# Performance work log

Measured on AMD Instinct MI355X. Metric: run time of the kernel, lower is better.

The kernel has to match this reference:

```python
import jax, jax.numpy as jnp
import numpy as np

D = 256      # d_model
H = 8        # n_heads
L = 4        # n_levels
P = 4        # n_points
DFF = 1024   # d_ffn
DH = D // H  # head dim
SPATIAL = np.array([[100, 100], [50, 50], [25, 25], [13, 13]], dtype=np.int64)  # (H_l, W_l)
LV = int((SPATIAL[:, 0] * SPATIAL[:, 1]).sum())  # 13294 flattened memory tokens


def layer_norm(x, w, b, eps=1e-5):
    m = jnp.mean(x, -1, keepdims=True)
    v = jnp.mean((x - m) ** 2, -1, keepdims=True)
    return (x - m) * jax.lax.rsqrt(v + eps) * w + b


def setup_inputs() -> dict:
    key = jax.random.key(0)
    ks = jax.random.split(key, 16)
    nq, bs = 900, 8

    def w(k, shape, s=0.02):
        return jax.random.normal(k, shape, dtype=jnp.float32) * s

    return {
        "tgt": jax.random.normal(ks[0], (nq, bs, D), jnp.float32),
        "tgt_query_pos": jax.random.normal(ks[1], (nq, bs, D), jnp.float32),
        "tgt_reference_points": jax.random.uniform(ks[2], (nq, bs, L, 2), jnp.float32),
        "memory": jax.random.normal(ks[3], (LV, bs, D), jnp.float32),
        "sa_Wqkv": w(ks[4], (3 * D, D)), "sa_bqkv": jnp.zeros((3 * D,), jnp.float32),
        "sa_Wo": w(ks[5], (D, D)), "sa_bo": jnp.zeros((D,), jnp.float32),
        "ln1_w": jnp.ones((D,), jnp.float32), "ln1_b": jnp.zeros((D,), jnp.float32),
        "ln2_w": jnp.ones((D,), jnp.float32), "ln2_b": jnp.zeros((D,), jnp.float32),
        "ln3_w": jnp.ones((D,), jnp.float32), "ln3_b": jnp.zeros((D,), jnp.float32),
        "ca_Woff": w(ks[6], (H * L * P * 2, D)), "ca_boff": w(ks[7], (H * L * P * 2,), 0.5),
        "ca_Wattn": w(ks[8], (H * L * P, D)), "ca_battn": jnp.zeros((H * L * P,), jnp.float32),
        "ca_Wval": w(ks[9], (D, D)), "ca_bval": jnp.zeros((D,), jnp.float32),
        "ca_Wout": w(ks[10], (D, D)), "ca_bout": jnp.zeros((D,), jnp.float32),
        "ffn_W1": w(ks[11], (DFF, D)), "ffn_b1": jnp.zeros((DFF,), jnp.float32),
        "ffn_W2": w(ks[12], (D, DFF)), "ffn_b2": jnp.zeros((D,), jnp.float32),
        "memory_key_padding_mask": jnp.zeros((bs, LV), jnp.bool_),
        "memory_spatial_shapes": jnp.asarray(SPATIAL),
    }


def msdeform_attn(query, ref, value, mask, shapes_np,
                  Woff, boff, Wattn, battn, Wval, bval, Wout, bout):
    # query: [bs,nq,D], ref: [bs,nq,L,2], value: [bs,lv,D], mask: [bs,lv]
    bs, nq, _ = query.shape
    lv = value.shape[1]
    v = value @ Wval.T + bval
    v = jnp.where(mask[:, :, None], 0.0, v)
    v = v.reshape(bs, lv, H, DH).transpose(0, 2, 1, 3)  # [bs,H,lv,DH]
    off = (query @ Woff.T + boff).reshape(bs, nq, H, L, P, 2)
    aw = jax.nn.softmax((query @ Wattn.T + battn).reshape(bs, nq, H, L * P), -1)
    aw = aw.reshape(bs, nq, H, L, P)
    # offset normalizer is [W_l, H_l]
    norm = jnp.asarray(shapes_np[:, ::-1].copy(), jnp.float32)  # [L,2]
    loc = ref[:, :, None, :, None, :] + off / norm[None, None, None, :, None, :]
    out = jnp.zeros((bs, nq, H, DH), jnp.float32)
    start = 0
    for l in range(L):
        Hl, Wl = int(shapes_np[l, 0]), int(shapes_np[l, 1])
        vf = v[:, :, start:start + Hl * Wl]  # [bs,H,Hl*Wl,DH]
        start += Hl * Wl
        # grid_sample(align_corners=False) pixel coords
        x = loc[:, :, :, l, :, 0] * Wl - 0.5  # [bs,nq,H,P]
        y = loc[:, :, :, l, :, 1] * Hl - 0.5
        x0 = jnp.floor(x); y0 = jnp.floor(y)
        fx = x - x0; fy = y - y0
        x0i = x0.astype(jnp.int32); y0i = y0.astype(jnp.int32)

        def gather(yi, xi):
            valid = ((xi >= 0) & (xi < Wl) & (yi >= 0) & (yi < Hl)).astype(jnp.float32)
            idx = jnp.clip(yi, 0, Hl - 1) * Wl + jnp.clip(xi, 0, Wl - 1)
            idx_t = idx.transpose(0, 2, 1, 3).reshape(bs, H, nq * P, 1)
            g = jnp.take_along_axis(vf, idx_t, axis=2)  # [bs,H,nq*P,DH]
            return g * valid.transpose(0, 2, 1, 3).reshape(bs, H, nq * P, 1)

        def wgt(w):
            return w.transpose(0, 2, 1, 3).reshape(bs, H, nq * P, 1)

        samp = (gather(y0i, x0i) * wgt((1 - fx) * (1 - fy))
                + gather(y0i, x0i + 1) * wgt(fx * (1 - fy))
                + gather(y0i + 1, x0i) * wgt((1 - fx) * fy)
                + gather(y0i + 1, x0i + 1) * wgt(fx * fy))
        samp = samp.reshape(bs, H, nq, P, DH)
        out = out + jnp.einsum('bhqpd,bqhp->bqhd', samp, aw[:, :, :, l])
    return out.reshape(bs, nq, D) @ Wout.T + bout


def reference(tgt, tgt_query_pos, tgt_reference_points, memory,
              sa_Wqkv, sa_bqkv, sa_Wo, sa_bo,
              ln1_w, ln1_b, ln2_w, ln2_b, ln3_w, ln3_b,
              ca_Woff, ca_boff, ca_Wattn, ca_battn, ca_Wval, ca_bval, ca_Wout, ca_bout,
              ffn_W1, ffn_b1, ffn_W2, ffn_b2,
              memory_key_padding_mask, memory_spatial_shapes):
    shapes_np = np.asarray(memory_spatial_shapes)  # static per trace
    nq, bs, _ = tgt.shape
    # --- self attention (post-LN, residual) ---
    q = tgt + tgt_query_pos
    qp = (q @ sa_Wqkv[:D].T + sa_bqkv[:D]).reshape(nq, bs, H, DH)
    kp = (q @ sa_Wqkv[D:2 * D].T + sa_bqkv[D:2 * D]).reshape(nq, bs, H, DH)
    vp = (tgt @ sa_Wqkv[2 * D:].T + sa_bqkv[2 * D:]).reshape(nq, bs, H, DH)
    scores = jnp.einsum('qbhd,kbhd->bhqk', qp, kp) * (1.0 / float(np.sqrt(DH)))
    attn = jax.nn.softmax(scores, -1)
    o = jnp.einsum('bhqk,kbhd->qbhd', attn, vp).reshape(nq, bs, D) @ sa_Wo.T + sa_bo
    tgt = layer_norm(tgt + o, ln2_w, ln2_b)
    # --- multi-scale deformable cross attention ---
    query = (tgt + tgt_query_pos).transpose(1, 0, 2)      # [bs,nq,D]
    ref = tgt_reference_points.transpose(1, 0, 2, 3)      # [bs,nq,L,2]
    val = memory.transpose(1, 0, 2)                       # [bs,lv,D]
    ca = msdeform_attn(query, ref, val, memory_key_padding_mask, shapes_np,
                       ca_Woff, ca_boff, ca_Wattn, ca_battn,
                       ca_Wval, ca_bval, ca_Wout, ca_bout).transpose(1, 0, 2)
    tgt = layer_norm(tgt + ca, ln1_w, ln1_b)
    # --- FFN ---
    t2 = jax.nn.relu(tgt @ ffn_W1.T + ffn_b1) @ ffn_W2.T + ffn_b2
    return layer_norm(tgt + t2, ln3_w, ln3_b)
```

## Files before the change

kernel.cpp:

```cpp
#include <hip/hip_runtime.h>
#include <hip/hip_bf16.h>

#define NQ   900
#define BSZ  8
#define DM   256
#define NH   8
#define DHD  32
#define DFF_ 1024
#define LVTOT 13294
#define NTOK (NQ*BSZ)
#define MVAL (LVTOT*BSZ)

typedef __attribute__((ext_vector_type(8))) short bf16x8;
typedef __attribute__((ext_vector_type(4))) short bf16x4;
typedef __attribute__((ext_vector_type(4))) float f32x4;
typedef unsigned int u32;

__device__ __forceinline__ unsigned short f2bf(float x) {
  union { __hip_bfloat16 h; unsigned short u; } cv;
  cv.h = __float2bfloat16(x);
  return cv.u;
}
__device__ __forceinline__ float bf2f(unsigned short u) {
  union { __hip_bfloat16 h; unsigned short u; } cv;
  cv.u = u;
  return __bfloat162float(cv.h);
}

__device__ __forceinline__ void gl_lds16(const void* gsrc, void* ldst) {
  __builtin_amdgcn_global_load_lds(
      (const __attribute__((address_space(1))) u32*)gsrc,
      (__attribute__((address_space(3))) u32*)ldst, 16, 0, 0);
}

__global__ __launch_bounds__(256) void addcast_kernel(const float* __restrict__ a,
                                                      const float* __restrict__ b,
                                                      unsigned short* __restrict__ o, int n8) {
  int i = blockIdx.x * 256 + threadIdx.x;
  if (i >= n8) return;
  float4 a0 = ((const float4*)a)[i * 2], a1 = ((const float4*)a)[i * 2 + 1];
  float4 b0 = ((const float4*)b)[i * 2], b1 = ((const float4*)b)[i * 2 + 1];
  bf16x8 v;
  v[0] = (short)f2bf(a0.x + b0.x); v[1] = (short)f2bf(a0.y + b0.y);
  v[2] = (short)f2bf(a0.z + b0.z); v[3] = (short)f2bf(a0.w + b0.w);
  v[4] = (short)f2bf(a1.x + b1.x); v[5] = (short)f2bf(a1.y + b1.y);
  v[6] = (short)f2bf(a1.z + b1.z); v[7] = (short)f2bf(a1.w + b1.w);
  *(bf16x8*)(o + (long)i * 8) = v;
}

__global__ __launch_bounds__(256) void cast_weights_kernel(
    const float* p0, const float* p1, const float* p2, const float* p3,
    const float* p4, const float* p5, const float* p6, const float* p7,
    unsigned short* dst) {
  long i8 = ((long)blockIdx.x * 256 + threadIdx.x) * 8;
  if (i8 >= 1015808) return;
  const float* src; long off;
  if      (i8 < 196608) { src = p0; off = i8; }
  else if (i8 < 262144) { src = p1; off = i8 - 196608; }
  else if (i8 < 327680) { src = p2; off = i8 - 262144; }
  else if (i8 < 393216) { src = p3; off = i8 - 327680; }
  else if (i8 < 425984) { src = p4; off = i8 - 393216; }
  else if (i8 < 491520) { src = p5; off = i8 - 425984; }
  else if (i8 < 753664) { src = p6; off = i8 - 491520; }
  else                  { src = p7; off = i8 - 753664; }
  float4 a = *(const float4*)(src + off);
  float4 b = *(const float4*)(src + off + 4);
  bf16x8 v;
  v[0] = (short)f2bf(a.x); v[1] = (short)f2bf(a.y);
  v[2] = (short)f2bf(a.z); v[3] = (short)f2bf(a.w);
  v[4] = (short)f2bf(b.x); v[5] = (short)f2bf(b.y);
  v[6] = (short)f2bf(b.z); v[7] = (short)f2bf(b.w);
  *(bf16x8*)(dst + i8) = v;
}

__global__ __launch_bounds__(256) void concat_bias_kernel(const float* __restrict__ a,
                                                          const float* __restrict__ b,
                                                          float* __restrict__ o) {
  int i = blockIdx.x * 256 + threadIdx.x;
  if (i < 256) o[i] = a[i];
  else if (i < 384) o[i] = b[i - 256];
}

template <int AF32, int OUT_BF16, int RELU, int NT>
__global__ __launch_bounds__(256) void gemm_mfma_kernel(
    const void* __restrict__ Araw, const unsigned short* __restrict__ W,
    const float* __restrict__ bias, void* __restrict__ C,
    int M, int ldc) {
  constexpr int K = NT * 32;
  constexpr int ABYTES = AF32 ? 16384 : 8192;
  __shared__ alignas(16) unsigned char As0[ABYTES];
  __shared__ alignas(16) unsigned char As1[ABYTES];
  __shared__ alignas(16) unsigned char As2[ABYTES];
  __shared__ alignas(16) unsigned char Bs0[8192];
  __shared__ alignas(16) unsigned char Bs1[8192];
  __shared__ alignas(16) unsigned char Bs2[8192];
  int tid = threadIdx.x;
  int l = tid & 63, w = tid >> 6;
  int lr = l & 15, lg = l >> 4;
  int wr = w >> 1, wc = w & 1;
  int n0 = blockIdx.x * 128, m0 = blockIdx.y * 128;

  f32x4 acc[4][4];
#pragma unroll
  for (int m = 0; m < 4; m++)
#pragma unroll
    for (int n = 0; n < 4; n++) acc[m][n] = (f32x4){0.f, 0.f, 0.f, 0.f};

  auto stage = [&](unsigned char* Ab, unsigned char* Bb, int k0) {
#pragma unroll
    for (int i = 0; i < 2; i++) {
      int c16 = i * 4 + w;
      int row = c16 * 16 + (l >> 2);
      int sc = (l & 3) ^ (row & 3);
      gl_lds16(W + (long)(n0 + row) * K + k0 + sc * 8, Bb + c16 * 1024 + l * 16);
    }
    if (AF32) {
      const float* Af = (const float*)Araw;
#pragma unroll
      for (int i = 0; i < 4; i++) {
        int c8 = i * 4 + w;
        int row = c8 * 8 + (l >> 3);
        int g = m0 + row; if (g >= M) g = M - 1;
        int sc = (l & 7) ^ (row & 7);
        gl_lds16(Af + (long)g * K + k0 + sc * 4, Ab + c8 * 1024 + l * 16);
      }
    } else {
      const unsigned short* A = (const unsigned short*)Araw;
#pragma unroll
      for (int i = 0; i < 2; i++) {
        int c16 = i * 4 + w;
        int row = c16 * 16 + (l >> 2);
        int g = m0 + row; if (g >= M) g = M - 1;
        int sc = (l & 3) ^ (row & 3);
        gl_lds16(A + (long)g * K + k0 + sc * 8, Ab + c16 * 1024 + l * 16);
      }
    }
  };

  auto compute = [&](const unsigned char* Ab, const unsigned char* Bb) {
    bf16x8 af[4], bfr[4];
    if (AF32) {
#pragma unroll
      for (int m = 0; m < 4; m++) {
        int row = wr * 64 + m * 16 + lr;
        f32x4 fa = *(const f32x4*)(Ab + row * 128 + (((lg * 2)     ^ (lr & 7)) * 16));
        f32x4 fb = *(const f32x4*)(Ab + row * 128 + (((lg * 2 + 1) ^ (lr & 7)) * 16));
        bf16x8 v;
        v[0] = (short)f2bf(fa[0]); v[1] = (short)f2bf(fa[1]);
        v[2] = (short)f2bf(fa[2]); v[3] = (short)f2bf(fa[3]);
        v[4] = (short)f2bf(fb[0]); v[5] = (short)f2bf(fb[1]);
        v[6] = (short)f2bf(fb[2]); v[7] = (short)f2bf(fb[3]);
        af[m] = v;
      }
    } else {
#pragma unroll
      for (int m = 0; m < 4; m++) {
        int row = wr * 64 + m * 16 + lr;
        af[m] = *(const bf16x8*)(Ab + row * 64 + ((lg ^ (lr & 3)) * 16));
      }
    }
#pragma unroll
    for (int n = 0; n < 4; n++) {
      int row = wc * 64 + n * 16 + lr;
      bfr[n] = *(const bf16x8*)(Bb + row * 64 + ((lg ^ (lr & 3)) * 16));
    }
#pragma unroll
    for (int m = 0; m < 4; m++)
#pragma unroll
      for (int n = 0; n < 4; n++)
        acc[m][n] = __builtin_amdgcn_mfma_f32_16x16x32_bf16(af[m], bfr[n], acc[m][n], 0, 0, 0);
  };

  unsigned char* Abuf[3] = {As0, As1, As2};
  unsigned char* Bbuf[3] = {Bs0, Bs1, Bs2};
  stage(As0, Bs0, 0);
  stage(As1, Bs1, 32);
  stage(As2, Bs2, 64);

#pragma unroll
  for (int t = 0; t < NT; t++) {
    const int ahead = NT - 1 - t;
    if (ahead >= 2) {
      if (AF32) asm volatile("s_waitcnt vmcnt(12)" ::: "memory");
      else      asm volatile("s_waitcnt vmcnt(8)"  ::: "memory");
    } else if (ahead == 1) {
      if (AF32) asm volatile("s_waitcnt vmcnt(6)" ::: "memory");
      else      asm volatile("s_waitcnt vmcnt(4)" ::: "memory");
    } else {
      asm volatile("s_waitcnt vmcnt(0)" ::: "memory");
    }
    __builtin_amdgcn_s_barrier();
    __builtin_amdgcn_sched_barrier(0);
    compute(Abuf[t % 3], Bbuf[t % 3]);
    __builtin_amdgcn_sched_barrier(0);
    __builtin_amdgcn_s_barrier();
    __builtin_amdgcn_sched_barrier(0);
    if (t + 3 < NT) stage(Abuf[t % 3], Bbuf[t % 3], (t + 3) * 32);
  }

  float bv[4];
#pragma unroll
  for (int ni = 0; ni < 4; ni++) bv[ni] = bias[n0 + wc * 64 + ni * 16 + lr];
#pragma unroll
  for (int mi = 0; mi < 4; mi++) {
#pragma unroll
    for (int r = 0; r < 4; r++) {
      int row = m0 + wr * 64 + mi * 16 + lg * 4 + r;
      if (row < M) {
#pragma unroll
        for (int ni = 0; ni < 4; ni++) {
          int col = n0 + wc * 64 + ni * 16 + lr;
          float v = acc[mi][ni][r] + bv[ni];
          if (RELU) v = fmaxf(v, 0.f);
          if (OUT_BF16) ((unsigned short*)C)[(long)row * ldc + col] = f2bf(v);
          else          ((float*)C)[(long)row * ldc + col] = v;
        }
      }
    }
  }
}

__global__ __launch_bounds__(256) void attn_mfma_kernel(const unsigned short* __restrict__ qkv,
                                                        unsigned short* __restrict__ out) {
  __shared__ unsigned short Vt[32][72];
  __shared__ unsigned short Ps[4][16][72];
  int tid = threadIdx.x;
  int l = tid & 63, w = tid >> 6;
  int lr = l & 15, lg = l >> 4;
  int q0 = blockIdx.x * 64;
  int h = blockIdx.y & 7, b = blockIdx.y >> 3;
  const float scale = 0.17677669529663687f;

  int qrow = q0 + w * 16 + lr;
  int qclamp = qrow < 899 ? qrow : 899;
  bf16x8 qf = *(const bf16x8*)(qkv + ((long)qclamp * 8 + b) * 768 + h * 32 + lg * 8);

  f32x4 o_acc[2];
  o_acc[0] = (f32x4){0.f, 0.f, 0.f, 0.f};
  o_acc[1] = (f32x4){0.f, 0.f, 0.f, 0.f};
  float m_run[4] = {-1e30f, -1e30f, -1e30f, -1e30f};
  float l_run[4] = {0.f, 0.f, 0.f, 0.f};

  for (int k0 = 0; k0 < NQ; k0 += 64) {
    __syncthreads();
    {
      int key = tid >> 2, dg = tid & 3;
      int kk = k0 + key; if (kk > 899) kk = 899;
      bf16x8 vv = *(const bf16x8*)(qkv + ((long)kk * 8 + b) * 768 + 512 + h * 32 + dg * 8);
#pragma unroll
      for (int j = 0; j < 8; j++) Vt[dg * 8 + j][key] = (unsigned short)vv[j];
    }
    f32x4 sg[4];
#pragma unroll
    for (int ng = 0; ng < 4; ng++) {
      int key = k0 + ng * 16 + lr; int kc = key < 899 ? key : 899;
      bf16x8 kf = *(const bf16x8*)(qkv + ((long)kc * 8 + b) * 768 + 256 + h * 32 + lg * 8);
      sg[ng] = __builtin_amdgcn_mfma_f32_16x16x32_bf16(qf, kf, (f32x4){0.f, 0.f, 0.f, 0.f}, 0, 0, 0);
    }
    float sv[4][4];
#pragma unroll
    for (int ng = 0; ng < 4; ng++) {
      bool bad = (k0 + ng * 16 + lr) >= NQ;
#pragma unroll
      for (int r = 0; r < 4; r++) sv[ng][r] = bad ? -1e30f : sg[ng][r] * scale;
    }
    float p[4][4];
#pragma unroll
    for (int r = 0; r < 4; r++) {
      float rmax = fmaxf(fmaxf(sv[0][r], sv[1][r]), fmaxf(sv[2][r], sv[3][r]));
#pragma unroll
      for (int mk = 8; mk; mk >>= 1) rmax = fmaxf(rmax, __shfl_xor(rmax, mk));
      float mnew = fmaxf(m_run[r], rmax);
      float fs = __expf(m_run[r] - mnew);
      m_run[r] = mnew;
      float ps = 0.f;
#pragma unroll
      for (int ng = 0; ng < 4; ng++) { p[ng][r] = __expf(sv[ng][r] - mnew); ps += p[ng][r]; }
#pragma unroll
      for (int mk = 8; mk; mk >>= 1) ps += __shfl_xor(ps, mk);
      l_run[r] = l_run[r] * fs + ps;
      o_acc[0][r] *= fs;
      o_acc[1][r] *= fs;
    }
#pragma unroll
    for (int ng = 0; ng < 4; ng++)
#pragma unroll
      for (int r = 0; r < 4; r++)
        Ps[w][lg * 4 + r][lr + ng * 16] = f2bf(p[ng][r]);
    __syncthreads();
#pragma unroll
    for (int ks = 0; ks < 2; ks++) {
      bf16x8 pf = *(const bf16x8*)&Ps[w][lr][ks * 32 + lg * 8];
#pragma unroll
      for (int ni = 0; ni < 2; ni++) {
        bf16x8 vf = *(const bf16x8*)&Vt[ni * 16 + lr][ks * 32 + lg * 8];
        o_acc[ni] = __builtin_amdgcn_mfma_f32_16x16x32_bf16(pf, vf, o_acc[ni], 0, 0, 0);
      }
    }
  }
#pragma unroll
  for (int r = 0; r < 4; r++) {
    int orow = q0 + w * 16 + lg * 4 + r;
    if (orow < NQ) {
      float inv = 1.f / l_run[r];
      unsigned short* op = out + ((long)orow * 8 + b) * 256 + h * 32 + lr;
      op[0]  = f2bf(o_acc[0][r] * inv);
      op[16] = f2bf(o_acc[1][r] * inv);
    }
  }
}

__device__ __forceinline__ void fetch8_acc(const unsigned short* __restrict__ vtmp, int lo, int W,
                                           int yi, int xi, int b, int col0, float wgt,
                                           float* a) {
  if ((xi < 0) | (xi >= W) | (yi < 0) | (yi >= W)) return;
  const unsigned short* p = vtmp + ((long)((lo + yi * W + xi) * BSZ + b)) * 256 + col0;
  bf16x8 r = *(const bf16x8*)p;
#pragma unroll
  for (int j = 0; j < 8; j++) a[j] += wgt * bf2f((unsigned short)r[j]);
}

__global__ __launch_bounds__(256) void sampler_kernel(const unsigned short* __restrict__ vtmp,
                                                      const float* __restrict__ oa,
                                                      const float* __restrict__ ref,
                                                      unsigned short* __restrict__ samp) {
  __shared__ float s_off[8][256];
  __shared__ float s_aw[8][128];
  __shared__ float s_ref[8][8];
  int tid = threadIdx.x;
  int t0 = blockIdx.x * 8;
#pragma unroll
  for (int k = 0; k < 8; k++) s_off[k][tid] = oa[(long)(t0 + k) * 384 + tid];
#pragma unroll
  for (int i = 0; i < 4; i++) {
    int idx = i * 256 + tid;
    int k = idx >> 7, c = idx & 127;
    s_aw[k][c] = oa[(long)(t0 + k) * 384 + 256 + c];
  }
  if (tid < 64) s_ref[tid >> 3][tid & 7] = ref[(long)(t0 + (tid >> 3)) * 8 + (tid & 7)];
  __syncthreads();
  if (tid < 64) {
    int k = tid >> 3, hh = tid & 7;
    float* p = &s_aw[k][hh * 16];
    float m = -1e30f;
#pragma unroll
    for (int j = 0; j < 16; j++) m = fmaxf(m, p[j]);
    float s = 0.f;
#pragma unroll
    for (int j = 0; j < 16; j++) { p[j] = __expf(p[j] - m); s += p[j]; }
    float inv = 1.f / s;
#pragma unroll
    for (int j = 0; j < 16; j++) p[j] *= inv;
  }
  __syncthreads();
  int w = tid >> 5;
  int l = tid & 31;
  int t = t0 + w;
  int h = l >> 2, col0 = h * 32 + (l & 3) * 8;
  int b = t & 7;
  const int Wls[4]  = {100, 50, 25, 13};
  const int lofs[4] = {0, 10000, 12500, 13125};
  float a[8];
#pragma unroll
  for (int j = 0; j < 8; j++) a[j] = 0.f;
#pragma unroll
  for (int lvl = 0; lvl < 4; lvl++) {
    int W = Wls[lvl];
    float Wf = (float)W;
    int lo = lofs[lvl];
    float rx = s_ref[w][lvl * 2 + 0], ry = s_ref[w][lvl * 2 + 1];
#pragma unroll
    for (int p = 0; p < 4; p++) {
      float ox = s_off[w][((h * 4 + lvl) * 4 + p) * 2 + 0];
      float oy = s_off[w][((h * 4 + lvl) * 4 + p) * 2 + 1];
      float x = rx * Wf + ox - 0.5f;
      float y = ry * Wf + oy - 0.5f;
      float x0f = floorf(x), y0f = floorf(y);
      float fx = x - x0f, fy = y - y0f;
      int x0 = (int)x0f, y0 = (int)y0f;
      float aa = s_aw[w][h * 16 + lvl * 4 + p];
      float w00 = aa * (1.f - fx) * (1.f - fy);
      float w01 = aa * fx * (1.f - fy);
      float w10 = aa * (1.f - fx) * fy;
      float w11 = aa * fx * fy;
      fetch8_acc(vtmp, lo, W, y0,     x0,     b, col0, w00, a);
      fetch8_acc(vtmp, lo, W, y0,     x0 + 1, b, col0, w01, a);
      fetch8_acc(vtmp, lo, W, y0 + 1, x0,     b, col0, w10, a);
      fetch8_acc(vtmp, lo, W, y0 + 1, x0 + 1, b, col0, w11, a);
    }
  }
  bf16x8 o;
#pragma unroll
  for (int j = 0; j < 8; j++) o[j] = (short)f2bf(a[j]);
  *(bf16x8*)(samp + (long)t * 256 + col0) = o;
}

__global__ __launch_bounds__(256) void ln_kernel(const float* __restrict__ x,
                                                 const float* __restrict__ res,
                                                 const float* __restrict__ w,
                                                 const float* __restrict__ bvec,
                                                 float* __restrict__ out,
                                                 unsigned short* __restrict__ out_bf,
                                                 const float* __restrict__ pos,
                                                 unsigned short* __restrict__ pos_bf,
                                                 int rows) {
  int wv = threadIdx.x >> 6, lane = threadIdx.x & 63;
  int row = blockIdx.x * 4 + wv;
  if (row >= rows) return;
  float4 xv = *(const float4*)(x + (long)row * 256 + lane * 4);
  float4 rv = *(const float4*)(res + (long)row * 256 + lane * 4);
  float v0 = xv.x + rv.x, v1 = xv.y + rv.y, v2 = xv.z + rv.z, v3 = xv.w + rv.w;
  float s = v0 + v1 + v2 + v3;
#pragma unroll
  for (int o = 32; o; o >>= 1) s += __shfl_xor(s, o);
  float mean = s * (1.f / 256.f);
  float d0 = v0 - mean, d1 = v1 - mean, d2 = v2 - mean, d3 = v3 - mean;
  float q = d0 * d0 + d1 * d1 + d2 * d2 + d3 * d3;
#pragma unroll
  for (int o = 32; o; o >>= 1) q += __shfl_xor(q, o);
  float rstd = rsqrtf(q * (1.f / 256.f) + 1e-5f);
  float4 wv4 = *(const float4*)(w + lane * 4);
  float4 bv4 = *(const float4*)(bvec + lane * 4);
  float o0 = d0 * rstd * wv4.x + bv4.x;
  float o1 = d1 * rstd * wv4.y + bv4.y;
  float o2 = d2 * rstd * wv4.z + bv4.z;
  float o3 = d3 * rstd * wv4.w + bv4.w;
  *(float4*)(out + (long)row * 256 + lane * 4) = make_float4(o0, o1, o2, o3);
  if (out_bf) {
    unsigned short* p = out_bf + (long)row * 256 + lane * 4;
    p[0] = f2bf(o0); p[1] = f2bf(o1); p[2] = f2bf(o2); p[3] = f2bf(o3);
  }
  if (pos_bf) {
    float4 pv = *(const float4*)(pos + (long)row * 256 + lane * 4);
    unsigned short* p = pos_bf + (long)row * 256 + lane * 4;
    p[0] = f2bf(o0 + pv.x); p[1] = f2bf(o1 + pv.y);
    p[2] = f2bf(o2 + pv.z); p[3] = f2bf(o3 + pv.w);
  }
}

extern "C" void kernel_launch(void* const* d_in, const int* in_sizes, int n_in,
                              void* d_out, int out_size, void* d_ws, size_t ws_size,
                              hipStream_t stream) {
  const float* tgt     = (const float*)d_in[0];
  const float* pos     = (const float*)d_in[1];
  const float* refpts  = (const float*)d_in[2];
  const float* memory  = (const float*)d_in[3];
  const float* sa_Wqkv = (const float*)d_in[4];
  const float* sa_bqkv = (const float*)d_in[5];
  const float* sa_Wo   = (const float*)d_in[6];
  const float* sa_bo   = (const float*)d_in[7];
  const float* ln1_w   = (const float*)d_in[8];
  const float* ln1_b   = (const float*)d_in[9];
  const float* ln2_w   = (const float*)d_in[10];
  const float* ln2_b   = (const float*)d_in[11];
  const float* ln3_w   = (const float*)d_in[12];
  const float* ln3_b   = (const float*)d_in[13];
  const float* ca_Woff = (const float*)d_in[14];
  const float* ca_boff = (const float*)d_in[15];
  const float* ca_Wattn= (const float*)d_in[16];
  const float* ca_battn= (const float*)d_in[17];
  const float* ca_Wval = (const float*)d_in[18];
  const float* ca_bval = (const float*)d_in[19];
  const float* ca_Wout = (const float*)d_in[20];
  const float* ca_bout = (const float*)d_in[21];
  const float* ffn_W1  = (const float*)d_in[22];
  const float* ffn_b1  = (const float*)d_in[23];
  const float* ffn_W2  = (const float*)d_in[24];
  const float* ffn_b2  = (const float*)d_in[25];

  char* ws = (char*)d_ws;
  float*          buf_ca = (float*)(ws);
  float*          buf_t3 = (float*)(ws + 8388608);
  unsigned short* t3_bf  = (unsigned short*)(ws + 16777216);
  unsigned short* buf_h  = (unsigned short*)(ws + 20971520);
  float*          buf_f  = (float*)(ws + 36700160);
  float*          bias_cat = (float*)(ws + 44072960);
  unsigned short* buf_v  = (unsigned short*)(ws + 54452224);
  unsigned short* wts    = (unsigned short*)(ws + 112590848);
  unsigned short* buf_q  = (unsigned short*)(ws + 114622464);
  unsigned short* buf_qkv= (unsigned short*)(ws + 118308864);
  float*          buf_oa = (float*)(ws + 118308864);
  unsigned short* buf_o  = (unsigned short*)(ws + 129368064);
  unsigned short* buf_smp= (unsigned short*)(ws + 129368064);
  float*          buf_t2 = (float*)(ws + 133054464);

  const unsigned short* w_qkv = wts + 0;
  const unsigned short* w_o   = wts + 196608;
  const unsigned short* w_val = wts + 262144;
  const unsigned short* w_oa  = wts + 327680;
  const unsigned short* w_out = wts + 425984;
  const unsigned short* w_f1  = wts + 491520;
  const unsigned short* w_f2  = wts + 753664;

  dim3 blk(256);
  const int n8tok = NTOK * DM / 8;

  cast_weights_kernel<<<(1015808 / 8 + 255) / 256, blk, 0, stream>>>(
      sa_Wqkv, sa_Wo, ca_Wval, ca_Woff, ca_Wattn, ca_Wout, ffn_W1, ffn_W2, wts);
  concat_bias_kernel<<<2, blk, 0, stream>>>(ca_boff, ca_battn, bias_cat);
  addcast_kernel<<<(n8tok + 255) / 256, blk, 0, stream>>>(tgt, pos, buf_q, n8tok);
  gemm_mfma_kernel<0, 1, 0, 8><<<dim3(4, 57), blk, 0, stream>>>(buf_q, w_qkv, sa_bqkv,
                                                                buf_qkv, NTOK, 768);
  gemm_mfma_kernel<1, 1, 0, 8><<<dim3(2, 57), blk, 0, stream>>>(tgt, w_qkv + 512 * 256,
                                                                sa_bqkv + 512, buf_qkv + 512,
                                                                NTOK, 768);
  gemm_mfma_kernel<1, 1, 0, 8><<<dim3(2, 831), blk, 0, stream>>>(memory, w_val, ca_bval,
                                                                 buf_v, MVAL, 256);
  attn_mfma_kernel<<<dim3(15, 64), blk, 0, stream>>>(buf_qkv, buf_o);
  gemm_mfma_kernel<0, 0, 0, 8><<<dim3(2, 57), blk, 0, stream>>>(buf_o, w_o, sa_bo,
                                                                buf_t2, NTOK, 256);
  ln_kernel<<<1800, blk, 0, stream>>>(buf_t2, tgt, ln2_w, ln2_b, buf_t2, nullptr,
                                      pos, buf_q, NTOK);
  gemm_mfma_kernel<0, 0, 0, 8><<<dim3(3, 57), blk, 0, stream>>>(buf_q, w_oa, bias_cat,
                                                                buf_oa, NTOK, 384);
  sampler_kernel<<<NTOK / 8, blk, 0, stream>>>(buf_v, buf_oa, refpts, buf_smp);
  gemm_mfma_kernel<0, 0, 0, 8><<<dim3(2, 57), blk, 0, stream>>>(buf_smp, w_out, ca_bout,
                                                                buf_ca, NTOK, 256);
  ln_kernel<<<1800, blk, 0, stream>>>(buf_ca, buf_t2, ln1_w, ln1_b, buf_t3, t3_bf,
                                      nullptr, nullptr, NTOK);
  gemm_mfma_kernel<0, 1, 1, 8><<<dim3(8, 57), blk, 0, stream>>>(t3_bf, w_f1, ffn_b1,
                                                                buf_h, NTOK, 1024);
  gemm_mfma_kernel<0, 0, 0, 32><<<dim3(2, 57), blk, 0, stream>>>(buf_h, w_f2, ffn_b2,
                                                                 buf_f, NTOK, 256);
  ln_kernel<<<1800, blk, 0, stream>>>(buf_f, buf_t3, ln3_w, ln3_b, (float*)d_out, nullptr,
                                      nullptr, nullptr, NTOK);
}
```

Measured before the change: 234.9 us.

## Add K=256 GEMM kernel that preloads all weights to LDS and streams A

Introduces a GEMM kernel specialised for K=256 that loads the full 128x256 weight tile into LDS once, then reads A fragments directly from global memory into registers, with no A staging in LDS and no per-k-step barriers. It replaces the triple-buffered LDS pipeline for all K=256 GEMMs, including the large memory value projection. The aim is to remove the synchronisation and LDS traffic for A. The cost is 64KB of LDS per block, which limits occupancy, and uncoalesced direct global A loads whose latency is no longer hidden by a software pipeline.

```diff
diff --git a/kernel.cpp b/kernel.cpp
--- a/kernel.cpp
+++ b/kernel.cpp
@@ -79,6 +79,102 @@
   int i = blockIdx.x * 256 + threadIdx.x;
   if (i < 256) o[i] = a[i];
   else if (i < 384) o[i] = b[i - 256];
+}
+
+template <int AF32, int OUT_BF16, int RELU>
+__global__ __launch_bounds__(256, 2) void gemm_stream_kernel(
+    const void* __restrict__ Araw, const unsigned short* __restrict__ W,
+    const float* __restrict__ bias, void* __restrict__ C,
+    int M, int ldc) {
+  __shared__ alignas(16) unsigned char Bp[8][8192];
+  int tid = threadIdx.x;
+  int l = tid & 63, w = tid >> 6;
+  int lr = l & 15, lg = l >> 4;
+  int wr = w >> 1, wc = w & 1;
+  int n0 = blockIdx.x * 128, m0 = blockIdx.y * 128;
+
+#pragma unroll
+  for (int kt = 0; kt < 8; kt++) {
+#pragma unroll
+    for (int i = 0; i < 2; i++) {
+      int c16 = i * 4 + w;
+      int row = c16 * 16 + (l >> 2);
+      int sc = (l & 3) ^ (row & 3);
+      gl_lds16(W + (long)(n0 + row) * 256 + kt * 32 + sc * 8, Bp[kt] + c16 * 1024 + l * 16);
+    }
+  }
+
+  f32x4 acc[4][4];
+#pragma unroll
+  for (int m = 0; m < 4; m++)
+#pragma unroll
+    for (int n = 0; n < 4; n++) acc[m][n] = (f32x4){0.f, 0.f, 0.f, 0.f};
+
+  long arow[4];
+#pragma unroll
+  for (int m = 0; m < 4; m++) {
+    long r = m0 + wr * 64 + m * 16 + lr;
+    arow[m] = (r < M) ? r : (M - 1);
+  }
+
+  __syncthreads();
+
+#pragma unroll
+  for (int kt = 0; kt < 8; kt++) {
+    bf16x8 af[4];
+    if (AF32) {
+      const float* Af = (const float*)Araw;
+#pragma unroll
+      for (int m = 0; m < 4; m++) {
+        const float* p = Af + arow[m] * 256 + kt * 32 + lg * 8;
+        f32x4 fa = *(const f32x4*)p;
+        f32x4 fb = *(const f32x4*)(p + 4);
+        bf16x8 v;
+        v[0] = (short)f2bf(fa[0]); v[1] = (short)f2bf(fa[1]);
+        v[2] = (short)f2bf(fa[2]); v[3] = (short)f2bf(fa[3]);
+        v[4] = (short)f2bf(fb[0]); v[5] = (short)f2bf(fb[1]);
+        v[6] = (short)f2bf(fb[2]); v[7] = (short)f2bf(fb[3]);
+        af[m] = v;
+      }
+    } else {
+      const unsigned short* A = (const unsigned short*)Araw;
+#pragma unroll
+      for (int m = 0; m < 4; m++)
+        af[m] = *(const bf16x8*)(A + arow[m] * 256 + kt * 32 + lg * 8);
+    }
+    bf16x8 bfr[4];
+#pragma unroll
+    for (int n = 0; n < 4; n++) {
+      int row = wc * 64 + n * 16 + lr;
+      bfr[n] = *(const bf16x8*)(Bp[kt] + (row >> 4) * 1024 + ((row & 15) * 4 + (lg ^ (row & 3))) * 16);
+    }
+#pragma unroll
+    for (int m = 0; m < 4; m++)
+#pragma unroll
+      for (int n = 0; n < 4; n++)
+        acc[m][n] = __builtin_amdgcn_mfma_f32_16x16x32_bf16(af[m], bfr[n], acc[m][n], 0, 0, 0);
+  }
+
+  float bv[4];
+#pragma unroll
+  for (int ni = 0; ni < 4; ni++) bv[ni] = bias[n0 + wc * 64 + ni * 16 + lr];
+#pragma unroll
+  for (int mi = 0; mi < 4; mi++) {
+#pragma unroll
+    for (int r = 0; r < 4; r++) {
+      int row = m0 + wr * 64 + mi * 16 + lg * 4 + r;
+      if (row < M) {
+#pragma unroll
+        for (int ni = 0; ni < 4; ni++) {
+          int col = n0 + wc * 64 + ni * 16 + lr;
+          float v = acc[mi][ni][r] + bv[ni];
+          if (RELU) v = fmaxf(v, 0.f);
+          if (OUT_BF16) ((unsigned short*)C)[(long)row * ldc + col] = f2bf(v);
+          else          ((float*)C)[(long)row * ldc + col] = v;
+        }
+      }
+    }
+  }
 }
 
 template <int AF32, int OUT_BF16, int RELU, int NT>
@@ -499,27 +595,27 @@
       sa_Wqkv, sa_Wo, ca_Wval, ca_Woff, ca_Wattn, ca_Wout, ffn_W1, ffn_W2, wts);
   concat_bias_kernel<<<2, blk, 0, stream>>>(ca_boff, ca_battn, bias_cat);
   addcast_kernel<<<(n8tok + 255) / 256, blk, 0, stream>>>(tgt, pos, buf_q, n8tok);
-  gemm_mfma_kernel<0, 1, 0, 8><<<dim3(4, 57), blk, 0, stream>>>(buf_q, w_qkv, sa_bqkv,
-                                                                buf_qkv, NTOK, 768);
-  gemm_mfma_kernel<1, 1, 0, 8><<<dim3(2, 57), blk, 0, stream>>>(tgt, w_qkv + 512 * 256,
-                                                                sa_bqkv + 512, buf_qkv + 512,
-                                                                NTOK, 768);
-  gemm_mfma_kernel<1, 1, 0, 8><<<dim3(2, 831), blk, 0, stream>>>(memory, w_val, ca_bval,
-                                                                 buf_v, MVAL, 256);
+  gemm_stream_kernel<0, 1, 0><<<dim3(4, 57), blk, 0, stream>>>(buf_q, w_qkv, sa_bqkv,
+                                                               buf_qkv, NTOK, 768);
+  gemm_stream_kernel<1, 1, 0><<<dim3(2, 57), blk, 0, stream>>>(tgt, w_qkv + 512 * 256,
+                                                               sa_bqkv + 512, buf_qkv + 512,
+                                                               NTOK, 768);
+  gemm_stream_kernel<1, 1, 0><<<dim3(2, 831), blk, 0, stream>>>(memory, w_val, ca_bval,
+                                                                buf_v, MVAL, 256);
   attn_mfma_kernel<<<dim3(15, 64), blk, 0, stream>>>(buf_qkv, buf_o);
-  gemm_mfma_kernel<0, 0, 0, 8><<<dim3(2, 57), blk, 0, stream>>>(buf_o, w_o, sa_bo,
-                                                                buf_t2, NTOK, 256);
+  gemm_stream_kernel<0, 0, 0><<<dim3(2, 57), blk, 0, stream>>>(buf_o, w_o, sa_bo,
+                                                               buf_t2, NTOK, 256);
   ln_kernel<<<1800, blk, 0, stream>>>(buf_t2, tgt, ln2_w, ln2_b, buf_t2, nullptr,
                                       pos, buf_q, NTOK);
-  gemm_mfma_kernel<0, 0, 0, 8><<<dim3(3, 57), blk, 0, stream>>>(buf_q, w_oa, bias_cat,
-                                                                buf_oa, NTOK, 384);
+  gemm_stream_kernel<0, 0, 0><<<dim3(3, 57), blk, 0, stream>>>(buf_q, w_oa, bias_cat,
+                                                               buf_oa, NTOK, 384);
   sampler_kernel<<<NTOK / 8, blk, 0, stream>>>(buf_v, buf_oa, refpts, buf_smp);
-  gemm_mfma_kernel<0, 0, 0, 8><<<dim3(2, 57), blk, 0, stream>>>(buf_smp, w_out, ca_bout,
-                                                                buf_ca, NTOK, 256);
+  gemm_stream_kernel<0, 0, 0><<<dim3(2, 57), blk, 0, stream>>>(buf_smp, w_out, ca_bout,
+                                                               buf_ca, NTOK, 256);
   ln_kernel<<<1800, blk, 0, stream>>>(buf_ca, buf_t2, ln1_w, ln1_b, buf_t3, t3_bf,
                                       nullptr, nullptr, NTOK);
-  gemm_mfma_kernel<0, 1, 1, 8><<<dim3(8, 57), blk, 0, stream>>>(t3_bf, w_f1, ffn_b1,
-                                                                buf_h, NTOK, 1024);
+  gemm_stream_kernel<0, 1, 1><<<dim3(8, 57), blk, 0, stream>>>(t3_bf, w_f1, ffn_b1,
+                                                               buf_h, NTOK, 1024);
   gemm_mfma_kernel<0, 0, 0, 32><<<dim3(2, 57), blk, 0, stream>>>(buf_h, w_f2, ffn_b2,
                                                                  buf_f, NTOK, 256);
   ln_kernel<<<1800, blk, 0, stream>>>(buf_f, buf_t3, ln3_w, ln3_b, (float*)d_out, nullptr,
```

Measured after the change: 281.9 us. 1.2x slower.

## Replace triple-buffered GEMM pipeline with single-buffer 64-wide K steps

Applied to the files above, without the earlier changes.

The GEMM kernel drops its three-stage LDS ring buffer with hand-tuned vmcnt waits. It now uses one A/B buffer per block, loaded with K=64 per step and guarded by two __syncthreads per step, with __launch_bounds__(256,4) to raise occupancy. This trades intra-block load/compute overlap for more resident blocks and fewer barrier rounds, relying on other blocks to hide memory latency. The swizzle patterns are widened to 8/16 chunks to match the wider rows.

```diff
diff --git a/kernel.cpp b/kernel.cpp
--- a/kernel.cpp
+++ b/kernel.cpp
@@ -81,19 +81,15 @@
   else if (i < 384) o[i] = b[i - 256];
 }
 
-template <int AF32, int OUT_BF16, int RELU, int NT>
-__global__ __launch_bounds__(256) void gemm_mfma_kernel(
+template <int AF32, int OUT_BF16, int RELU, int NSTEP>
+__global__ __launch_bounds__(256, 4) void gemm_s_kernel(
     const void* __restrict__ Araw, const unsigned short* __restrict__ W,
     const float* __restrict__ bias, void* __restrict__ C,
     int M, int ldc) {
-  constexpr int K = NT * 32;
-  constexpr int ABYTES = AF32 ? 16384 : 8192;
-  __shared__ alignas(16) unsigned char As0[ABYTES];
-  __shared__ alignas(16) unsigned char As1[ABYTES];
-  __shared__ alignas(16) unsigned char As2[ABYTES];
-  __shared__ alignas(16) unsigned char Bs0[8192];
-  __shared__ alignas(16) unsigned char Bs1[8192];
-  __shared__ alignas(16) unsigned char Bs2[8192];
+  constexpr int K = NSTEP * 64;
+  constexpr int ABYTES = AF32 ? 32768 : 16384;
+  __shared__ alignas(16) unsigned char As[ABYTES];
+  __shared__ alignas(16) unsigned char Bs[16384];
   int tid = threadIdx.x;
   int l = tid & 63, w = tid >> 6;
   int lr = l & 15, lg = l >> 4;
@@ -106,96 +102,77 @@
 #pragma unroll
     for (int n = 0; n < 4; n++) acc[m][n] = (f32x4){0.f, 0.f, 0.f, 0.f};
 
-  auto stage = [&](unsigned char* Ab, unsigned char* Bb, int k0) {
-#pragma unroll
-    for (int i = 0; i < 2; i++) {
-      int c16 = i * 4 + w;
-      int row = c16 * 16 + (l >> 2);
-      int sc = (l & 3) ^ (row & 3);
-      gl_lds16(W + (long)(n0 + row) * K + k0 + sc * 8, Bb + c16 * 1024 + l * 16);
+  for (int t = 0; t < NSTEP; t++) {
+    int k0 = t * 64;
+    __syncthreads();
+#pragma unroll
+    for (int i4 = 0; i4 < 4; i4++) {
+      int i = i4 * 4 + w;
+      int row = i * 8 + (l >> 3);
+      int sc = (l & 7) ^ (row & 7);
+      gl_lds16(W + (long)(n0 + row) * K + k0 + sc * 8, Bs + i * 1024 + l * 16);
     }
     if (AF32) {
       const float* Af = (const float*)Araw;
 #pragma unroll
-      for (int i = 0; i < 4; i++) {
-        int c8 = i * 4 + w;
-        int row = c8 * 8 + (l >> 3);
+      for (int i4 = 0; i4 < 8; i4++) {
+        int i = i4 * 4 + w;
+        int row = i * 4 + (l >> 4);
         int g = m0 + row; if (g >= M) g = M - 1;
-        int sc = (l & 7) ^ (row & 7);
-        gl_lds16(Af + (long)g * K + k0 + sc * 4, Ab + c8 * 1024 + l * 16);
+        int sc = (l & 15) ^ (row & 15);
+        gl_lds16(Af + (long)g * K + k0 + sc * 4, As + i * 1024 + l * 16);
       }
     } else {
       const unsigned short* A = (const unsigned short*)Araw;
 #pragma unroll
-      for (int i = 0; i < 2; i++) {
-        int c16 = i * 4 + w;
-        int row = c16 * 16 + (l >> 2);
+      for (int i4 = 0; i4 < 4; i4++) {
+        int i = i4 * 4 + w;
+        int row = i * 8 + (l >> 3);
         int g = m0 + row; if (g >= M) g = M - 1;
-        int sc = (l & 3) ^ (row & 3);
-        gl_lds16(A + (long)g * K + k0 + sc * 8, Ab + c16 * 1024 + l * 16);
+        int sc = (l & 7) ^ (row & 7);
+        gl_lds16(A + (long)g * K + k0 + sc * 8, As + i * 1024 + l * 16);
       }
     }
-  };
-
-  auto compute = [&](const unsigned char* Ab, const unsigned char* Bb) {
-    bf16x8 af[4], bfr[4];
-    if (AF32) {
-#pragma unroll
-      for (int m = 0; m < 4; m++) {
-        int row = wr * 64 + m * 16 + lr;
-        f32x4 fa = *(const f32x4*)(Ab + row * 128 + (((lg * 2)     ^ (lr & 7)) * 16));
-        f32x4 fb = *(const f32x4*)(Ab + row * 128 + (((lg * 2 + 1) ^ (lr & 7)) * 16));
-        bf16x8 v;
-        v[0] = (short)f2bf(fa[0]); v[1] = (short)f2bf(fa[1]);
-        v[2] = (short)f2bf(fa[2]); v[3] = (short)f2bf(fa[3]);
-        v[4] = (short)f2bf(fb[0]); v[5] = (short)f2bf(fb[1]);
-        v[6] = (short)f2bf(fb[2]); v[7] = (short)f2bf(fb[3]);
-        af[m] = v;
+    __syncthreads();
+
+#pragma unroll
+    for (int sk = 0; sk < 2; sk++) {
+      bf16x8 af[4], bfr[4];
+      if (AF32) {
+#pragma unroll
+        for (int m = 0; m < 4; m++) {
+          int row = wr * 64 + m * 16 + lr;
+          int ca = (sk * 8 + lg * 2) ^ (row & 15);
+          int cb = (sk * 8 + lg * 2 + 1) ^ (row & 15);
+          f32x4 fa = *(const f32x4*)(As + row * 256 + ca * 16);
+          f32x4 fb = *(const f32x4*)(As + row * 256 + cb * 16);
+          bf16x8 v;
+          v[0] = (short)f2bf(fa[0]); v[1] = (short)f2bf(fa[1]);
+          v[2] = (short)f2bf(fa[2]); v[3] = (short)f2bf(fa[3]);
+          v[4] = (short)f2bf(fb[0]); v[5] = (short)f2bf(fb[1]);
+          v[6] = (short)f2bf(fb[2]); v[7] = (short)f2bf(fb[3]);
+          af[m] = v;
+        }
+      } else {
+#pragma unroll
+        for (int m = 0; m < 4; m++) {
+          int row = wr * 64 + m * 16 + lr;
+          int c = (sk * 4 + lg) ^ (row & 7);
+          af[m] = *(const bf16x8*)(As + row * 128 + c * 16);
+        }
       }
-    } else {
-#pragma unroll
-      for (int m = 0; m < 4; m++) {
-        int row = wr * 64 + m * 16 + lr;
-        af[m] = *(const bf16x8*)(Ab + row * 64 + ((lg ^ (lr & 3)) * 16));
+#pragma unroll
+      for (int n = 0; n < 4; n++) {
+        int row = wc * 64 + n * 16 + lr;
+        int c = (sk * 4 + lg) ^ (row & 7);
+        bfr[n] = *(const bf16x8*)(Bs + row * 128 + c * 16);
       }
-    }
-#pragma unroll
-    for (int n = 0; n < 4; n++) {
-      int row = wc * 64 + n * 16 + lr;
-      bfr[n] = *(const bf16x8*)(Bb + row * 64 + ((lg ^ (lr & 3)) * 16));
-    }
-#pragma unroll
-    for (int m = 0; m < 4; m++)
-#pragma unroll
-      for (int n = 0; n < 4; n++)
-        acc[m][n] = __builtin_amdgcn_mfma_f32_16x16x32_bf16(af[m], bfr[n], acc[m][n], 0, 0, 0);
-  };
-
-  unsigned char* Abuf[3] = {As0, As1, As2};
-  unsigned char* Bbuf[3] = {Bs0, Bs1, Bs2};
-  stage(As0, Bs0, 0);
-  stage(As1, Bs1, 32);
-  stage(As2, Bs2, 64);
-
-#pragma unroll
-  for (int t = 0; t < NT; t++) {
-    const int ahead = NT - 1 - t;
-    if (ahead >= 2) {
-      if (AF32) asm volatile("s_waitcnt vmcnt(12)" ::: "memory");
-      else      asm volatile("s_waitcnt vmcnt(8)"  ::: "memory");
-    } else if (ahead == 1) {
-      if (AF32) asm volatile("s_waitcnt vmcnt(6)" ::: "memory");
-      else      asm volatile("s_waitcnt vmcnt(4)" ::: "memory");
-    } else {
-      asm volatile("s_waitcnt vmcnt(0)" ::: "memory");
-    }
-    __builtin_amdgcn_s_barrier();
-    __builtin_amdgcn_sched_barrier(0);
-    compute(Abuf[t % 3], Bbuf[t % 3]);
-    __builtin_amdgcn_sched_barrier(0);
-    __builtin_amdgcn_s_barrier();
-    __builtin_amdgcn_sched_barrier(0);
-    if (t + 3 < NT) stage(Abuf[t % 3], Bbuf[t % 3], (t + 3) * 32);
+#pragma unroll
+      for (int m = 0; m < 4; m++)
+#pragma unroll
+        for (int n = 0; n < 4; n++)
+          acc[m][n] = __builtin_amdgcn_mfma_f32_16x16x32_bf16(af[m], bfr[n], acc[m][n], 0, 0, 0);
+    }
   }
 
   float bv[4];
@@ -499,29 +476,29 @@
       sa_Wqkv, sa_Wo, ca_Wval, ca_Woff, ca_Wattn, ca_Wout, ffn_W1, ffn_W2, wts);
   concat_bias_kernel<<<2, blk, 0, stream>>>(ca_boff, ca_battn, bias_cat);
   addcast_kernel<<<(n8tok + 255) / 256, blk, 0, stream>>>(tgt, pos, buf_q, n8tok);
-  gemm_mfma_kernel<0, 1, 0, 8><<<dim3(4, 57), blk, 0, stream>>>(buf_q, w_qkv, sa_bqkv,
-                                                                buf_qkv, NTOK, 768);
-  gemm_mfma_kernel<1, 1, 0, 8><<<dim3(2, 57), blk, 0, stream>>>(tgt, w_qkv + 512 * 256,
-                                                                sa_bqkv + 512, buf_qkv + 512,
-                                                                NTOK, 768);
-  gemm_mfma_kernel<1, 1, 0, 8><<<dim3(2, 831), blk, 0, stream>>>(memory, w_val, ca_bval,
-                                                                 buf_v, MVAL, 256);
+  gemm_s_kernel<0, 1, 0, 4><<<dim3(4, 57), blk, 0, stream>>>(buf_q, w_qkv, sa_bqkv,
+                                                             buf_qkv, NTOK, 768);
+  gemm_s_kernel<1, 1, 0, 4><<<dim3(2, 57), blk, 0, stream>>>(tgt, w_qkv + 512 * 256,
+                                                             sa_bqkv + 512, buf_qkv + 512,
+                                                             NTOK, 768);
+  gemm_s_kernel<1, 1, 0, 4><<<dim3(2, 831), blk, 0, stream>>>(memory, w_val, ca_bval,
+                                                              buf_v, MVAL, 256);
   attn_mfma_kernel<<<dim3(15, 64), blk, 0, stream>>>(buf_qkv, buf_o);
-  gemm_mfma_kernel<0, 0, 0, 8><<<dim3(2, 57), blk, 0, stream>>>(buf_o, w_o, sa_bo,
-                                                                buf_t2, NTOK, 256);
+  gemm_s_kernel<0, 0, 0, 4><<<dim3(2, 57), blk, 0, stream>>>(buf_o, w_o, sa_bo,
+                                                             buf_t2, NTOK, 256);
   ln_kernel<<<1800, blk, 0, stream>>>(buf_t2, tgt, ln2_w, ln2_b, buf_t2, nullptr,
                                       pos, buf_q, NTOK);
-  gemm_mfma_kernel<0, 0, 0, 8><<<dim3(3, 57), blk, 0, stream>>>(buf_q, w_oa, bias_cat,
-                                                                buf_oa, NTOK, 384);
+  gemm_s_kernel<0, 0, 0, 4><<<dim3(3, 57), blk, 0, stream>>>(buf_q, w_oa, bias_cat,
+                                                             buf_oa, NTOK, 384);
   sampler_kernel<<<NTOK / 8, blk, 0, stream>>>(buf_v, buf_oa, refpts, buf_smp);
-  gemm_mfma_kernel<0, 0, 0, 8><<<dim3(2, 57), blk, 0, stream>>>(buf_smp, w_out, ca_bout,
-                                                                buf_ca, NTOK, 256);
+  gemm_s_kernel<0, 0, 0, 4><<<dim3(2, 57), blk, 0, stream>>>(buf_smp, w_out, ca_bout,
+                                                             buf_ca, NTOK, 256);
   ln_kernel<<<1800, blk, 0, stream>>>(buf_ca, buf_t2, ln1_w, ln1_b, buf_t3, t3_bf,
                                       nullptr, nullptr, NTOK);
-  gemm_mfma_kernel<0, 1, 1, 8><<<dim3(8, 57), blk, 0, stream>>>(t3_bf, w_f1, ffn_b1,
-                                                                buf_h, NTOK, 1024);
-  gemm_mfma_kernel<0, 0, 0, 32><<<dim3(2, 57), blk, 0, stream>>>(buf_h, w_f2, ffn_b2,
-                                                                 buf_f, NTOK, 256);
+  gemm_s_kernel<0, 1, 1, 4><<<dim3(8, 57), blk, 0, stream>>>(t3_bf, w_f1, ffn_b1,
+                                                             buf_h, NTOK, 1024);
+  gemm_s_kernel<0, 0, 0, 16><<<dim3(2, 57), blk, 0, stream>>>(buf_h, w_f2, ffn_b2,
+                                                              buf_f, NTOK, 256);
   ln_kernel<<<1800, blk, 0, stream>>>(buf_f, buf_t3, ln3_w, ln3_b, (float*)d_out, nullptr,
                                       nullptr, nullptr, NTOK);
 }
```

Result: no change. 232.2 us (-1.2%).
